# Performance work log

Measured on AMD Instinct MI355X. Metric: run time of the kernel, lower is better.

## Reference

```python
import jax, jax.numpy as jnp
import numpy as np

NUM_CIRCLES = 7
B, D_IN, D_HID, D_OUT = 4096, 2048, 3584, 2048  # D_HID % 7 == 0 (7 * 512)


def setup_inputs() -> dict:
    key = jax.random.key(0)
    k1, k2, k3, k4 = jax.random.split(key, 4)
    x = jax.random.normal(k1, (B, D_IN), dtype=jnp.float32)
    # FlowerOfLife: 7 bias-free Linear(D_IN -> D_HID//7) weights, stacked [7, D_HID//7, D_IN]
    W_flower = jax.random.normal(k2, (NUM_CIRCLES, D_HID // NUM_CIRCLES, D_IN), dtype=jnp.float32) / np.sqrt(D_IN).astype(np.float32)
    # Merkaba: two bias-free Linear(D_HID -> D_OUT)
    W_male = jax.random.normal(k3, (D_OUT, D_HID), dtype=jnp.float32) / np.sqrt(D_HID).astype(np.float32)
    W_female = jax.random.normal(k4, (D_OUT, D_HID), dtype=jnp.float32) / np.sqrt(D_HID).astype(np.float32)
    return {"x": x, "W_flower": W_flower, "W_male": W_male, "W_female": W_female}


def reference(x, W_flower, W_male, W_female):
    # --- VesicaPiscisOperation: sacred overlap with the batch-rolled neighbor ---
    x2 = jnp.roll(x, 1, axis=0)
    dist = jnp.linalg.norm(x - x2, axis=1, keepdims=True)          # [B, 1]
    overlap = jax.nn.relu(1.0 - jnp.abs(dist - 1.0))               # [B, 1]
    x_overlap = x * (1.0 + overlap)                                # per-row scaling

    # --- FlowerOfLifeProjection: 7 parallel projections, phase-shift first 2 dims ---
    circ = jnp.einsum('bd,cod->bco', x_overlap, W_flower)          # [B, 7, D_HID//7]
    phases = 2.0 * jnp.pi * jnp.arange(NUM_CIRCLES, dtype=jnp.float32) / NUM_CIRCLES
    phase_shift = jnp.stack([jnp.cos(phases), jnp.sin(phases)], axis=-1)  # [7, 2]
    circ = circ.at[:, :, :2].multiply(phase_shift[None, :, :])
    x_expanded = circ.reshape(x.shape[0], -1)                      # [B, D_HID]

    # --- MerkabaRotation: counter-rotating transforms + sigmoid phase lock ---
    male = x_expanded @ W_male.T                                   # [B, D_OUT]
    female = x_expanded[:, ::-1] @ W_female.T                      # flip(-1) then Linear
    phase_lock = jax.nn.sigmoid(jnp.sum(male * female, axis=-1, keepdims=True))
    return phase_lock * male + (1.0 - phase_lock) * female
```

## Files before the change

### kernel.cpp

```cpp
#include <hip/hip_runtime.h>
#include <hip/hip_bf16.h>
#include <math.h>

#define B_DIM 4096
#define D_IN  2048
#define D_HID 3584
#define D_OUT 2048

typedef __bf16 bf16;
typedef float  floatx4 __attribute__((ext_vector_type(4)));
typedef bf16   bf16x8  __attribute__((ext_vector_type(8)));
typedef bf16   bf16x4  __attribute__((ext_vector_type(4)));

typedef __attribute__((address_space(1))) const void* gptr1;
typedef __attribute__((address_space(3))) void*       lptr3;

__device__ __forceinline__ void load_lds16(const void* g, void* l) {
    __builtin_amdgcn_global_load_lds((gptr1)g, (lptr3)l, 16, 0, 0);
}

struct HL { bf16 h, l; };
__device__ __forceinline__ HL split2(float v) {
    HL r;
    r.h = (bf16)v;
    r.l = (bf16)(v - (float)r.h);
    return r;
}

__device__ __forceinline__ void xcd_tile(int& n0, int& m0) {
    const int d  = (int)(blockIdx.x + gridDim.x * blockIdx.y);
    const int r  = d >> 3;
    const int nx = ((d & 7) << 1) | (r & 1);
    const int my = r >> 1;
    n0 = nx * 128;
    m0 = my * 128;
}

__global__ __launch_bounds__(256) void prep_kernel(const float* __restrict__ x,
                                                   const float* __restrict__ Wfl,
                                                   const float* __restrict__ Wm,
                                                   const float* __restrict__ Wfe,
                                                   bf16* __restrict__ xh,
                                                   bf16* __restrict__ xl,
                                                   bf16* __restrict__ th,
                                                   bf16* __restrict__ tl,
                                                   bf16* __restrict__ wh,
                                                   bf16* __restrict__ wl) {
    __shared__ float tile[64][65];
    const int id = blockIdx.x;
    const int t  = threadIdx.x;

    if (id < 4096) {
        const int b  = id;
        const int bp = (b == 0) ? (B_DIM - 1) : (b - 1);

        const floatx4* xr = (const floatx4*)(x + (size_t)b  * D_IN);
        const floatx4* pr = (const floatx4*)(x + (size_t)bp * D_IN);
        const floatx4 v0 = xr[t * 2], v1 = xr[t * 2 + 1];
        const floatx4 p0 = pr[t * 2], p1 = pr[t * 2 + 1];

        float s = 0.f;
#pragma unroll
        for (int j = 0; j < 4; ++j) {
            const float d0 = v0[j] - p0[j], d1 = v1[j] - p1[j];
            s += d0 * d0 + d1 * d1;
        }
#pragma unroll
        for (int off = 32; off > 0; off >>= 1) s += __shfl_down(s, off, 64);

        float* red = &tile[0][0];
        const int wave = t >> 6, lane = t & 63;
        if (lane == 0) red[wave] = s;
        __syncthreads();
        const float dist = sqrtf(red[0] + red[1] + red[2] + red[3]);
        const float sc   = 1.f + fmaxf(0.f, 1.f - fabsf(dist - 1.f));

        bf16x8 h, l;
#pragma unroll
        for (int j = 0; j < 4; ++j) {
            const HL a  = split2(v0[j] * sc);
            const HL b2 = split2(v1[j] * sc);
            h[j] = a.h;      l[j] = a.l;
            h[4 + j] = b2.h; l[4 + j] = b2.l;
        }
        ((bf16x8*)(xh + (size_t)b * D_IN))[t] = h;
        ((bf16x8*)(xl + (size_t)b * D_IN))[t] = l;

    } else if (id < 4096 + 1792) {
        const int tb = id - 4096;
        const int d0 = (tb & 31) << 6;
        const int h0 = (tb >> 5) << 6;
        const int r  = t >> 4;
        const int cg = (t & 15) << 2;

#pragma unroll
        for (int i = 0; i < 4; ++i) {
            const int hr = r + i * 16;
            const floatx4 v = *(const floatx4*)&Wfl[(size_t)(h0 + hr) * 2048 + d0 + cg];
            tile[hr][cg]     = v[0];
            tile[hr][cg + 1] = v[1];
            tile[hr][cg + 2] = v[2];
            tile[hr][cg + 3] = v[3];
        }
        __syncthreads();

        float pm[4];
#pragma unroll
        for (int j = 0; j < 4; ++j) {
            const int h  = h0 + cg + j;
            const int hm = h & 511;
            float p = 1.f;
            if (hm < 2) {
                const float ph = 0.8975979010256552f * (float)(h >> 9);
                p = (hm == 0) ? cosf(ph) : sinf(ph);
            }
            pm[j] = p;
        }

#pragma unroll
        for (int i = 0; i < 4; ++i) {
            const int dr = r + i * 16;
            bf16x4 hh, ll;
#pragma unroll
            for (int j = 0; j < 4; ++j) {
                const HL u = split2(tile[cg + j][dr] * pm[j]);
                hh[j] = u.h;
                ll[j] = u.l;
            }
            const size_t o = (size_t)(d0 + dr) * 3584 + h0 + cg;
            *(bf16x4*)&th[o] = hh;
            *(bf16x4*)&tl[o] = ll;
        }

    } else {
        const int i = (id - 5888) * 256 + t;
        const int o = i / 448;
        const int g = i - o * 448;
        bf16x8 h, l;
        if (o < 2048) {
            const float* src = Wm + (size_t)o * 3584 + (size_t)g * 8;
            const floatx4 a = ((const floatx4*)src)[0];
            const floatx4 b = ((const floatx4*)src)[1];
#pragma unroll
            for (int j = 0; j < 4; ++j) {
                const HL u = split2(a[j]);
                const HL v = split2(b[j]);
                h[j] = u.h;     l[j] = u.l;
                h[4 + j] = v.h; l[4 + j] = v.l;
            }
        } else {
            const float* src = Wfe + (size_t)(o - 2048) * 3584 + (size_t)(447 - g) * 8;
            const floatx4 a = ((const floatx4*)src)[0];
            const floatx4 b = ((const floatx4*)src)[1];
#pragma unroll
            for (int j = 0; j < 4; ++j) {
                const HL u = split2(b[3 - j]);
                const HL v = split2(a[3 - j]);
                h[j] = u.h;     l[j] = u.l;
                h[4 + j] = v.h; l[4 + j] = v.l;
            }
        }
        ((bf16x8*)wh)[i] = h;
        ((bf16x8*)wl)[i] = l;
    }
}

__global__ __launch_bounds__(256, 2) void gemm3_single(const bf16* __restrict__ Ah,
                                                       const bf16* __restrict__ Al,
                                                       const bf16* __restrict__ Bh,
                                                       const bf16* __restrict__ Bl,
                                                       bf16* __restrict__ C0,
                                                       bf16* __restrict__ C1,
                                                       int M, int N, int K) {
    __shared__ bf16 sAh[128 * 64], sAl[128 * 64];
    __shared__ bf16 sBh[128 * 64], sBl[128 * 64];

    const int tid  = threadIdx.x;
    const int wave = tid >> 6;
    const int lane = tid & 63;
    int n0, m0;
    xcd_tile(n0, m0);
    const int wm   = wave & 1;
    const int wn   = wave >> 1;

    floatx4 acc[4][4];
#pragma unroll
    for (int i = 0; i < 4; ++i)
#pragma unroll
        for (int j = 0; j < 4; ++j) acc[i][j] = (floatx4){0.f, 0.f, 0.f, 0.f};

    const int lr  = lane & 15;
    const int cc8 = (lane >> 4) << 3;
    const int sw  = lr & 7;

    for (int kt = 0; kt < K; kt += 64) {
#pragma unroll
        for (int i = 0; i < 4; ++i) {
            const int q = ((i * 4 + wave) << 6) + lane;
            const int r = q >> 3;
            const int c = (q & 7) ^ (r & 7);
            const int e = q << 3;
            const size_t ga = (size_t)(m0 + r) * K + kt + c * 8;
            const size_t gb = (size_t)(n0 + r) * K + kt + c * 8;
            load_lds16(&Ah[ga], &sAh[e]);
            load_lds16(&Al[ga], &sAl[e]);
            load_lds16(&Bh[gb], &sBh[e]);
            load_lds16(&Bl[gb], &sBl[e]);
        }
        __syncthreads();

#pragma unroll
        for (int ks = 0; ks < 2; ++ks) {
            const int cb = (ks << 2) + (cc8 >> 3);
            const int co = (cb ^ sw) << 3;
            bf16x8 ah[4], al[4], bh[4], bl[4];
#pragma unroll
            for (int mi = 0; mi < 4; ++mi) {
                const int off = ((wm * 64 + mi * 16 + lr) << 6) + co;
                ah[mi] = *(const bf16x8*)&sAh[off];
                al[mi] = *(const bf16x8*)&sAl[off];
            }
#pragma unroll
            for (int ni = 0; ni < 4; ++ni) {
                const int off = ((wn * 64 + ni * 16 + lr) << 6) + co;
                bh[ni] = *(const bf16x8*)&sBh[off];
                bl[ni] = *(const bf16x8*)&sBl[off];
            }

#pragma unroll
            for (int mi = 0; mi < 4; ++mi)
#pragma unroll
                for (int ni = 0; ni < 4; ++ni) {
                    acc[mi][ni] = __builtin_amdgcn_mfma_f32_16x16x32_bf16(
                        ah[mi], bh[ni], acc[mi][ni], 0, 0, 0);
                    acc[mi][ni] = __builtin_amdgcn_mfma_f32_16x16x32_bf16(
                        al[mi], bh[ni], acc[mi][ni], 0, 0, 0);
                    acc[mi][ni] = __builtin_amdgcn_mfma_f32_16x16x32_bf16(
                        ah[mi], bl[ni], acc[mi][ni], 0, 0, 0);
                }
        }
        __syncthreads();
    }

    const int rq = (lane >> 4) << 2;
    const int cl = lane & 15;
#pragma unroll
    for (int mi = 0; mi < 4; ++mi) {
#pragma unroll
        for (int ni = 0; ni < 4; ++ni) {
            const int col = n0 + wn * 64 + ni * 16 + cl;
#pragma unroll
            for (int r = 0; r < 4; ++r) {
                const int row = m0 + wm * 64 + mi * 16 + rq + r;
                const size_t idx = (size_t)row * N + col;
                const HL u = split2(acc[mi][ni][r]);
                C0[idx] = u.h;
                C1[idx] = u.l;
            }
        }
    }
}

__global__ __launch_bounds__(256, 2) void gemm3_dual(const bf16* __restrict__ Ah,
                                                     const bf16* __restrict__ Al,
                                                     const bf16* __restrict__ Bmh,
                                                     const bf16* __restrict__ Bml,
                                                     const bf16* __restrict__ Bfh,
                                                     const bf16* __restrict__ Bfl,
                                                     float* __restrict__ Cm,
                                                     float* __restrict__ Cf,
                                                     int M, int N, int K) {
    __shared__ bf16 sAh[4096], sAl[4096];
    __shared__ bf16 sMh[4096], sMl[4096];
    __shared__ bf16 sFh[4096], sFl[4096];

    const int tid  = threadIdx.x;
    const int wave = tid >> 6;
    const int lane = tid & 63;
    int n0, m0;
    xcd_tile(n0, m0);
    const int wm   = wave & 1;
    const int wn   = wave >> 1;

    floatx4 am[4][4], af[4][4];
#pragma unroll
    for (int i = 0; i < 4; ++i)
#pragma unroll
        for (int j = 0; j < 4; ++j) {
            am[i][j] = (floatx4){0.f, 0.f, 0.f, 0.f};
            af[i][j] = (floatx4){0.f, 0.f, 0.f, 0.f};
        }

    const int lr  = lane & 15;
    const int cc8 = (lane >> 4) << 3;
    const int cq  = cc8 >> 3;
    const int hsw = lr >> 1;

    for (int kt = 0; kt < K; kt += 32) {
#pragma unroll
        for (int i = 0; i < 2; ++i) {
            const int q = ((i * 4 + wave) << 6) + lane;
            const int p = q ^ ((q >> 3) & 7);
            const int r = p >> 2, c = p & 3;
            const int e = q << 3;
            const size_t ga = (size_t)(m0 + r) * K + kt + c * 8;
            const size_t gb = (size_t)(n0 + r) * K + kt + c * 8;
            load_lds16(&Ah[ga],  &sAh[e]);
            load_lds16(&Al[ga],  &sAl[e]);
            load_lds16(&Bmh[gb], &sMh[e]);
            load_lds16(&Bml[gb], &sMl[e]);
            load_lds16(&Bfh[gb], &sFh[e]);
            load_lds16(&Bfl[gb], &sFl[e]);
        }
        __syncthreads();

        bf16x8 ah[4], al[4];
#pragma unroll
        for (int mi = 0; mi < 4; ++mi) {
            const int ql  = ((wm * 64 + mi * 16 + lr) << 2) + cq;
            const int off = (ql ^ hsw) << 3;
            ah[mi] = *(const bf16x8*)&sAh[off];
            al[mi] = *(const bf16x8*)&sAl[off];
        }
#pragma unroll
        for (int ni = 0; ni < 4; ++ni) {
            const int ql  = ((wn * 64 + ni * 16 + lr) << 2) + cq;
            const int off = (ql ^ hsw) << 3;
            const bf16x8 mh = *(const bf16x8*)&sMh[off];
            const bf16x8 ml = *(const bf16x8*)&sMl[off];
            const bf16x8 fh = *(const bf16x8*)&sFh[off];
            const bf16x8 fl = *(const bf16x8*)&sFl[off];
#pragma unroll
            for (int mi = 0; mi < 4; ++mi) {
                am[mi][ni] = __builtin_amdgcn_mfma_f32_16x16x32_bf16(
                    ah[mi], mh, am[mi][ni], 0, 0, 0);
                am[mi][ni] = __builtin_amdgcn_mfma_f32_16x16x32_bf16(
                    al[mi], mh, am[mi][ni], 0, 0, 0);
                am[mi][ni] = __builtin_amdgcn_mfma_f32_16x16x32_bf16(
                    ah[mi], ml, am[mi][ni], 0, 0, 0);
                af[mi][ni] = __builtin_amdgcn_mfma_f32_16x16x32_bf16(
                    ah[mi], fh, af[mi][ni], 0, 0, 0);
                af[mi][ni] = __builtin_amdgcn_mfma_f32_16x16x32_bf16(
                    al[mi], fh, af[mi][ni], 0, 0, 0);
                af[mi][ni] = __builtin_amdgcn_mfma_f32_16x16x32_bf16(
                    ah[mi], fl, af[mi][ni], 0, 0, 0);
            }
        }
        __syncthreads();
    }

    const int rq = (lane >> 4) << 2;
    const int cl = lane & 15;
#pragma unroll
    for (int mi = 0; mi < 4; ++mi) {
#pragma unroll
        for (int ni = 0; ni < 4; ++ni) {
            const int col = n0 + wn * 64 + ni * 16 + cl;
#pragma unroll
            for (int r = 0; r < 4; ++r) {
                const int row = m0 + wm * 64 + mi * 16 + rq + r;
                const size_t idx = (size_t)row * N + col;
                Cm[idx] = am[mi][ni][r];
                Cf[idx] = af[mi][ni][r];
            }
        }
    }
}

__global__ __launch_bounds__(256) void combine_kernel(const float* __restrict__ male,
                                                      const float* __restrict__ female,
                                                      float* __restrict__ out) {
    const int b = blockIdx.x;
    const int t = threadIdx.x;

    const floatx4* m4 = (const floatx4*)(male   + (size_t)b * D_OUT);
    const floatx4* f4 = (const floatx4*)(female + (size_t)b * D_OUT);
    const floatx4 mv0 = m4[t * 2], mv1 = m4[t * 2 + 1];
    const floatx4 fv0 = f4[t * 2], fv1 = f4[t * 2 + 1];

    float s = 0.f;
#pragma unroll
    for (int j = 0; j < 4; ++j) s += mv0[j] * fv0[j] + mv1[j] * fv1[j];
#pragma unroll
    for (int off = 32; off > 0; off >>= 1) s += __shfl_down(s, off, 64);

    __shared__ float red[4];
    const int wave = t >> 6, lane = t & 63;
    if (lane == 0) red[wave] = s;
    __syncthreads();
    const float dot = red[0] + red[1] + red[2] + red[3];
    const float pl  = 1.f / (1.f + expf(-dot));

    floatx4 o0, o1;
#pragma unroll
    for (int j = 0; j < 4; ++j) {
        o0[j] = pl * mv0[j] + (1.f - pl) * fv0[j];
        o1[j] = pl * mv1[j] + (1.f - pl) * fv1[j];
    }
    floatx4* o4 = (floatx4*)(out + (size_t)b * D_OUT);
    o4[t * 2]     = o0;
    o4[t * 2 + 1] = o1;
}

extern "C" void kernel_launch(void* const* d_in, const int* in_sizes, int n_in,
                              void* d_out, int out_size, void* d_ws, size_t ws_size,
                              hipStream_t stream) {
    const float* x   = (const float*)d_in[0];
    const float* Wfl = (const float*)d_in[1];
    const float* Wm  = (const float*)d_in[2];
    const float* Wfe = (const float*)d_in[3];
    float* out = (float*)d_out;
    (void)in_sizes; (void)n_in; (void)out_size; (void)ws_size;

    char* ws = (char*)d_ws;
    bf16*  xo_hi   = (bf16*)(ws);
    bf16*  xo_lo   = (bf16*)(ws + 16777216);
    bf16*  Wc_hi   = (bf16*)(ws + 33554432);
    bf16*  Wc_lo   = (bf16*)(ws + 50331648);
    bf16*  WflT_hi = (bf16*)(ws + 67108864);
    bf16*  WflT_lo = (bf16*)(ws + 81788928);
    bf16*  Wcat_hi = (bf16*)(ws + 96468992);
    bf16*  Wcat_lo = (bf16*)(ws + 125829120);
    float* male    = (float*)(ws + 67108864);
    float* female  = (float*)(ws + 100663296);

    prep_kernel<<<13056, 256, 0, stream>>>(x, Wfl, Wm, Wfe,
                                           xo_hi, xo_lo,
                                           WflT_hi, WflT_lo,
                                           Wcat_hi, Wcat_lo);

    gemm3_single<<<dim3(D_IN / 128, (2 * D_OUT) / 128), 256, 0, stream>>>(
        Wcat_hi, Wcat_lo, WflT_hi, WflT_lo, Wc_hi, Wc_lo,
        2 * D_OUT, D_IN, D_HID);

    gemm3_dual<<<dim3(D_OUT / 128, B_DIM / 128), 256, 0, stream>>>(
        xo_hi, xo_lo,
        Wc_hi, Wc_lo,
        Wc_hi + (size_t)D_OUT * D_IN, Wc_lo + (size_t)D_OUT * D_IN,
        male, female, B_DIM, D_OUT, D_IN);

    combine_kernel<<<B_DIM, 256, 0, stream>>>(male, female, out);
}
```

Before: 485.5 us.

## Rewrite weight-fold GEMM with 8-wave 256x128 tiles and triple-buffered LDS pipeline

```diff
diff --git a/kernel.cpp b/kernel.cpp
--- a/kernel.cpp
+++ b/kernel.cpp
@@ -165,23 +165,26 @@
     }
 }
 
-__global__ __launch_bounds__(256, 2) void gemm3_single(const bf16* __restrict__ Ah,
-                                                       const bf16* __restrict__ Al,
-                                                       const bf16* __restrict__ Bh,
-                                                       const bf16* __restrict__ Bl,
-                                                       bf16* __restrict__ C0,
-                                                       bf16* __restrict__ C1,
-                                                       int M, int N, int K) {
-    __shared__ bf16 sAh[128 * 64], sAl[128 * 64];
-    __shared__ bf16 sBh[128 * 64], sBl[128 * 64];
+__global__ __launch_bounds__(512, 2) void gemm3_single8(const bf16* __restrict__ Ah,
+                                                        const bf16* __restrict__ Al,
+                                                        const bf16* __restrict__ Bh,
+                                                        const bf16* __restrict__ Bl,
+                                                        bf16* __restrict__ C0,
+                                                        bf16* __restrict__ C1,
+                                                        int M, int N, int K) {
+    __shared__ bf16 lds[3 * 24576];
 
     const int tid  = threadIdx.x;
     const int wave = tid >> 6;
     const int lane = tid & 63;
-    int n0, m0;
-    xcd_tile(n0, m0);
-    const int wm   = wave & 1;
-    const int wn   = wave >> 1;
+
+    const int d  = (int)(blockIdx.x + gridDim.x * blockIdx.y);
+    const int rr = d >> 3;
+    const int n0 = (((d & 7) << 1) | (rr & 1)) * 128;
+    const int m0 = (rr >> 1) * 256;
+
+    const int wm = wave >> 1;
+    const int wn = wave & 1;
 
     floatx4 acc[4][4];
 #pragma unroll
@@ -190,57 +193,105 @@
         for (int j = 0; j < 4; ++j) acc[i][j] = (floatx4){0.f, 0.f, 0.f, 0.f};
 
     const int lr  = lane & 15;
-    const int cc8 = (lane >> 4) << 3;
-    const int sw  = lr & 7;
-
-    for (int kt = 0; kt < K; kt += 64) {
-#pragma unroll
-        for (int i = 0; i < 4; ++i) {
-            const int q = ((i * 4 + wave) << 6) + lane;
-            const int r = q >> 3;
-            const int c = (q & 7) ^ (r & 7);
-            const int e = q << 3;
-            const size_t ga = (size_t)(m0 + r) * K + kt + c * 8;
-            const size_t gb = (size_t)(n0 + r) * K + kt + c * 8;
-            load_lds16(&Ah[ga], &sAh[e]);
-            load_lds16(&Al[ga], &sAl[e]);
-            load_lds16(&Bh[gb], &sBh[e]);
-            load_lds16(&Bl[gb], &sBl[e]);
-        }
-        __syncthreads();
-
-#pragma unroll
-        for (int ks = 0; ks < 2; ++ks) {
-            const int cb = (ks << 2) + (cc8 >> 3);
-            const int co = (cb ^ sw) << 3;
-            bf16x8 ah[4], al[4], bh[4], bl[4];
-#pragma unroll
-            for (int mi = 0; mi < 4; ++mi) {
-                const int off = ((wm * 64 + mi * 16 + lr) << 6) + co;
-                ah[mi] = *(const bf16x8*)&sAh[off];
-                al[mi] = *(const bf16x8*)&sAl[off];
-            }
+    const int cq  = lane >> 4;
+    const int hsw = lr >> 1;
+
+    auto stageA = [&](int h, int slot, int which) {
+        const int q = (which << 9) + tid;
+        const int p = q ^ ((q >> 3) & 7);
+        const int r = p >> 2, c = p & 3;
+        const size_t ga = (size_t)(m0 + r) * K + (h << 5) + c * 8;
+        bf16* base = &lds[slot * 24576];
+        load_lds16(&Ah[ga], base + (q << 3));
+        load_lds16(&Al[ga], base + 8192 + (q << 3));
+    };
+    auto stageB = [&](int h, int slot) {
+        const int q = tid;
+        const int p = q ^ ((q >> 3) & 7);
+        const int r = p >> 2, c = p & 3;
+        const size_t gb = (size_t)(n0 + r) * K + (h << 5) + c * 8;
+        bf16* base = &lds[slot * 24576 + 16384];
+        load_lds16(&Bh[gb], base + (q << 3));
+        load_lds16(&Bl[gb], base + 4096 + (q << 3));
+    };
+
+    auto halfstep = [&](int h, int slot, int slot2, bool issue) {
+        const bf16* pAh = &lds[slot * 24576];
+        const bf16* pAl = pAh + 8192;
+        const bf16* pBh = pAh + 16384;
+        const bf16* pBl = pAh + 20480;
+
+        bf16x8 Afh[4], Afl[4], Bfh[4], Bfl[4];
+
+        __builtin_amdgcn_s_barrier();
+        if (issue) { stageA(h + 2, slot2, 0); stageA(h + 2, slot2, 1); }
+#pragma unroll
+        for (int mi = 0; mi < 2; ++mi) {
+            const int ql  = ((wm * 64 + mi * 16 + lr) << 2) + cq;
+            const int off = (ql ^ hsw) << 3;
+            Afh[mi] = *(const bf16x8*)&pAh[off];
+            Afl[mi] = *(const bf16x8*)&pAl[off];
+        }
+#pragma unroll
+        for (int ni = 0; ni < 4; ++ni) {
+            const int ql  = ((wn * 64 + ni * 16 + lr) << 2) + cq;
+            const int off = (ql ^ hsw) << 3;
+            Bfh[ni] = *(const bf16x8*)&pBh[off];
+            Bfl[ni] = *(const bf16x8*)&pBl[off];
+        }
+        __builtin_amdgcn_s_setprio(1);
+#pragma unroll
+        for (int mi = 0; mi < 2; ++mi)
 #pragma unroll
             for (int ni = 0; ni < 4; ++ni) {
-                const int off = ((wn * 64 + ni * 16 + lr) << 6) + co;
-                bh[ni] = *(const bf16x8*)&sBh[off];
-                bl[ni] = *(const bf16x8*)&sBl[off];
-            }
-
-#pragma unroll
-            for (int mi = 0; mi < 4; ++mi)
-#pragma unroll
-                for (int ni = 0; ni < 4; ++ni) {
-                    acc[mi][ni] = __builtin_amdgcn_mfma_f32_16x16x32_bf16(
-                        ah[mi], bh[ni], acc[mi][ni], 0, 0, 0);
-                    acc[mi][ni] = __builtin_amdgcn_mfma_f32_16x16x32_bf16(
-                        al[mi], bh[ni], acc[mi][ni], 0, 0, 0);
-                    acc[mi][ni] = __builtin_amdgcn_mfma_f32_16x16x32_bf16(
-                        ah[mi], bl[ni], acc[mi][ni], 0, 0, 0);
-                }
-        }
-        __syncthreads();
-    }
+                acc[mi][ni] = __builtin_amdgcn_mfma_f32_16x16x32_bf16(
+                    Afh[mi], Bfh[ni], acc[mi][ni], 0, 0, 0);
+                acc[mi][ni] = __builtin_amdgcn_mfma_f32_16x16x32_bf16(
+                    Afl[mi], Bfh[ni], acc[mi][ni], 0, 0, 0);
+                acc[mi][ni] = __builtin_amdgcn_mfma_f32_16x16x32_bf16(
+                    Afh[mi], Bfl[ni], acc[mi][ni], 0, 0, 0);
+            }
+        __builtin_amdgcn_s_setprio(0);
+        __builtin_amdgcn_s_barrier();
+        if (issue) stageB(h + 2, slot2);
+#pragma unroll
+        for (int mi = 2; mi < 4; ++mi) {
+            const int ql  = ((wm * 64 + mi * 16 + lr) << 2) + cq;
+            const int off = (ql ^ hsw) << 3;
+            Afh[mi] = *(const bf16x8*)&pAh[off];
+            Afl[mi] = *(const bf16x8*)&pAl[off];
+        }
+        __builtin_amdgcn_s_setprio(1);
+#pragma unroll
+        for (int mi = 2; mi < 4; ++mi)
+#pragma unroll
+            for (int ni = 0; ni < 4; ++ni) {
+                acc[mi][ni] = __builtin_amdgcn_mfma_f32_16x16x32_bf16(
+                    Afh[mi], Bfh[ni], acc[mi][ni], 0, 0, 0);
+                acc[mi][ni] = __builtin_amdgcn_mfma_f32_16x16x32_bf16(
+                    Afl[mi], Bfh[ni], acc[mi][ni], 0, 0, 0);
+                acc[mi][ni] = __builtin_amdgcn_mfma_f32_16x16x32_bf16(
+                    Afh[mi], Bfl[ni], acc[mi][ni], 0, 0, 0);
+            }
+        __builtin_amdgcn_s_setprio(0);
+    };
+
+    stageA(0, 0, 0); stageA(0, 0, 1); stageB(0, 0);
+    stageA(1, 1, 0); stageA(1, 1, 1); stageB(1, 1);
+
+    const int NH = K >> 5;
+    int slot = 0, slot2 = 2;
+    for (int h = 0; h < NH - 2; ++h) {
+        asm volatile("s_waitcnt vmcnt(6)" ::: "memory");
+        halfstep(h, slot, slot2, true);
+        slot  = (slot  == 2) ? 0 : slot + 1;
+        slot2 = (slot2 == 2) ? 0 : slot2 + 1;
+    }
+    asm volatile("s_waitcnt vmcnt(6)" ::: "memory");
+    halfstep(NH - 2, slot, slot2, false);
+    slot = (slot == 2) ? 0 : slot + 1;
+    asm volatile("s_waitcnt vmcnt(0)" ::: "memory");
+    halfstep(NH - 1, slot, slot2, false);
 
     const int rq = (lane >> 4) << 2;
     const int cl = lane & 15;
@@ -429,7 +480,7 @@
                                            WflT_hi, WflT_lo,
                                            Wcat_hi, Wcat_lo);
 
-    gemm3_single<<<dim3(D_IN / 128, (2 * D_OUT) / 128), 256, 0, stream>>>(
+    gemm3_single8<<<dim3(16, 16), 512, 0, stream>>>(
         Wcat_hi, Wcat_lo, WflT_hi, WflT_lo, Wc_hi, Wc_lo,
         2 * D_OUT, D_IN, D_HID);
 
```

Result: no change. 488.4 us (+0.6%).
